# Performance work log

Hardware: AMD Instinct MI355X
Metric: run time of the kernel (lower is better)

Reference implementation:

```python
import jax, jax.numpy as jnp
import numpy as np

N = 50000          # nodes
E = 800000         # edges (avg degree 16)
DIN = 128          # d_input
H = 8              # heads per layer
D = 16             # per-head hidden dim
HID = H * D        # 128
ALPHA = 0.2        # LeakyReLU negative slope in GAT attention
BN_EPS = 1e-5


def _xavier(key, shape):
    fan_in, fan_out = shape[0], shape[-1]
    lim = np.sqrt(6.0 / (fan_in + fan_out)).astype(np.float32)
    return jax.random.uniform(key, shape, jnp.float32, -lim, lim)


def setup_inputs() -> dict:
    key = jax.random.key(0)
    ks = jax.random.split(key, 8)
    x = jax.random.normal(ks[0], (N, DIN), jnp.float32)
    edge_idx = jax.random.randint(ks[1], (2, E), 0, N)
    W1 = _xavier(ks[2], (DIN, HID))
    a1 = _xavier(ks[3], (H, 2 * D))
    W2 = _xavier(ks[4], (HID, HID))
    a2 = _xavier(ks[5], (H, 2 * D))
    W3 = _xavier(ks[6], (HID, HID))
    a3 = _xavier(ks[7], (H, 2 * D))
    ones = jnp.ones((HID,), jnp.float32)
    zeros = jnp.zeros((HID,), jnp.float32)
    return {"x": x, "edge_idx": edge_idx,
            "W1": W1, "a1": a1, "W2": W2, "a2": a2, "W3": W3, "a3": a3,
            "g1": ones, "b1": zeros, "g2": ones, "b2": zeros, "g3": ones, "b3": zeros}


def _leaky(x):
    return jnp.where(x >= 0, x, ALPHA * x)


def _gat_layer(x, src, dst, W, a):
    # x: [N, Fin]; W: [Fin, H*D]; a: [H, 2D]
    h = (x @ W).reshape(-1, H, D)                       # [N, H, D]
    e_src = jnp.einsum('nhd,hd->nh', h, a[:, :D])       # a^T part for source node
    e_dst = jnp.einsum('nhd,hd->nh', h, a[:, D:])       # a^T part for destination node
    e = _leaky(e_src[src] + e_dst[dst])                 # [E, H]
    m = jax.ops.segment_max(e, dst, num_segments=N)     # per-dst stable softmax max
    m = jnp.where(jnp.isfinite(m), m, 0.0)              # empty segments -> 0
    w = jnp.exp(e - m[dst])                             # [E, H]
    den = jax.ops.segment_sum(w, dst, num_segments=N)   # [N, H]
    agg = jax.ops.segment_sum(h[src] * w[:, :, None], dst, num_segments=N)  # [N, H, D]
    out = agg / (den[:, :, None] + 1e-16)
    return out.reshape(-1, HID)                         # concat heads


def _bn(x, g, b):
    # BatchNorm1d training-mode math over the node axis
    mu = x.mean(axis=0)
    var = x.var(axis=0)
    return g * (x - mu) * jax.lax.rsqrt(var + BN_EPS) + b


def reference(x, edge_idx, W1, a1, W2, a2, W3, a3, g1, b1, g2, b2, g3, b3):
    src, dst = edge_idx[0], edge_idx[1]
    h1 = jax.nn.elu(_bn(_gat_layer(x, src, dst, W1, a1), g1, b1))
    h2 = jax.nn.elu(_bn(_gat_layer(h1, src, dst, W2, a2), g2, b2))
    h3_in = h1 + h2  # skip connection
    return _bn(_gat_layer(h3_in, src, dst, W3, a3), g3, b3)
```

## Files before the change

kernel.cpp:

```cpp
#include <hip/hip_runtime.h>
#include <hip/hip_bf16.h>
#include <hip/hip_fp16.h>
#include <cstddef>

#define NNODES 50000
#define NEDGES 800000
#define HID 128
#define NHEAD 8
#define AGG_NB (NNODES / 16)
#define NSLICE 64
#define SLAYER (NSLICE * 512)

#define NBUCK 196
#define BCH 2048
#define BIN_NB ((NEDGES + BCH - 1) / BCH)

typedef __attribute__((ext_vector_type(4))) float floatx4;
typedef _Float16 __attribute__((ext_vector_type(8))) half8;
typedef _Float16 __attribute__((ext_vector_type(2))) half2v;

static inline size_t align_up(size_t x, size_t a) { return (x + a - 1) & ~(a - 1); }

__device__ inline float fexp2(float x) {
#if __has_builtin(__builtin_amdgcn_exp2f)
    return __builtin_amdgcn_exp2f(x);
#else
    return __expf(x * 0.69314718055994531f);
#endif
}

__device__ inline unsigned short f2h(float f) {
    return __builtin_bit_cast(unsigned short, (_Float16)f);
}

__global__ __launch_bounds__(256) void init_kernel(const float* __restrict__ W1,
                                                   const float* __restrict__ W2,
                                                   const float* __restrict__ W3,
                                                   unsigned short* __restrict__ Wt,
                                                   int* __restrict__ zeroA, int nA,
                                                   float* __restrict__ zeroB, int nB) {
    int b = blockIdx.x;
    int t = threadIdx.x;
    if (b < 192) {
        int layer = b >> 6;
        const float* W = (layer == 0) ? W1 : ((layer == 1) ? W2 : W3);
        int idx = (b & 63) * 256 + t;
        int n = idx & 127;
        int k = idx >> 7;
        Wt[layer * 16384 + n * 128 + k] = f2h(W[idx]);
    } else {
        int nb = gridDim.x - 192;
        int bb = b - 192;
        for (int i = bb * 256 + t; i < nA; i += nb * 256) zeroA[i] = 0;
        for (int i = bb * 256 + t; i < nB; i += nb * 256) zeroB[i] = 0.f;
    }
}

__global__ __launch_bounds__(256) void bin_count_kernel(const int* __restrict__ edge,
                                                        int* __restrict__ bucketCnt) {
    __shared__ int h[NBUCK];
    int t = threadIdx.x;
    if (t < NBUCK) h[t] = 0;
    __syncthreads();
    for (int i = blockIdx.x * 256 + t; i < NEDGES; i += gridDim.x * 256)
        atomicAdd(&h[edge[NEDGES + i] >> 8], 1);
    __syncthreads();
    if (t < NBUCK && h[t]) atomicAdd(&bucketCnt[t], h[t]);
}

__global__ __launch_bounds__(256) void bucket_scan_kernel(const int* __restrict__ bucketCnt,
                                                          int* __restrict__ bucketBase) {
    __shared__ int sA[256];
    int t = threadIdx.x;
    int v = (t < NBUCK) ? bucketCnt[t] : 0;
    sA[t] = v;
    __syncthreads();
    for (int off = 1; off < 256; off <<= 1) {
        int x = (t >= off) ? sA[t - off] : 0;
        __syncthreads();
        sA[t] += x;
        __syncthreads();
    }
    if (t < NBUCK) bucketBase[t] = sA[t] - v;
    if (t == 0) bucketBase[NBUCK] = NEDGES;
}

__global__ __launch_bounds__(256) void bin_scatter_kernel(const int* __restrict__ edge,
                                                          const int* __restrict__ bucketBase,
                                                          int* __restrict__ bucketCursor,
                                                          unsigned int* __restrict__ binned) {
    __shared__ int sA[256];
    __shared__ int hcnt[NBUCK];
    __shared__ int hbase[NBUCK];
    __shared__ int gbase[NBUCK];
    __shared__ unsigned int sEnt[BCH];
    __shared__ unsigned char sBk[BCH];
    int t = threadIdx.x;
    int e0 = blockIdx.x * BCH;
    int nv = NEDGES - e0;
    if (nv > BCH) nv = BCH;

    if (t < NBUCK) hcnt[t] = 0;
    __syncthreads();

    int myB[8];
    int myR[8];
    unsigned int myP[8];
    #pragma unroll
    for (int j = 0; j < 8; ++j) {
        int idx = j * 256 + t;
        myB[j] = -1;
        if (idx < nv) {
            int s = edge[e0 + idx];
            int d = edge[NEDGES + e0 + idx];
            int bk = d >> 8;
            myB[j] = bk;
            myP[j] = (unsigned)s | ((unsigned)(d & 255) << 16);
            myR[j] = atomicAdd(&hcnt[bk], 1);
        }
    }
    __syncthreads();
    int hc = (t < NBUCK) ? hcnt[t] : 0;
    sA[t] = hc;
    __syncthreads();
    for (int off = 1; off < 256; off <<= 1) {
        int x = (t >= off) ? sA[t - off] : 0;
        __syncthreads();
        sA[t] += x;
        __syncthreads();
    }
    if (t < NBUCK) {
        hbase[t] = sA[t] - hc;
        gbase[t] = bucketBase[t] + atomicAdd(&bucketCursor[t], hc);
    }
    __syncthreads();
    #pragma unroll
    for (int j = 0; j < 8; ++j) {
        if (myB[j] >= 0) {
            int p = hbase[myB[j]] + myR[j];
            sEnt[p] = myP[j];
            sBk[p] = (unsigned char)myB[j];
        }
    }
    __syncthreads();
    #pragma unroll
    for (int j = 0; j < 8; ++j) {
        int i = j * 256 + t;
        if (i < nv) {
            int bk = sBk[i];
            binned[gbase[bk] + (i - hbase[bk])] = sEnt[i];
        }
    }
}

__global__ __launch_bounds__(256) void fine_csr_kernel(const int* __restrict__ bucketCnt,
                                                       const int* __restrict__ bucketBase,
                                                       const unsigned int* __restrict__ binned,
                                                       int* __restrict__ offs,
                                                       int* __restrict__ csr) {
    __shared__ int sA[256];
    __shared__ int sB[256];
    int t = threadIdx.x;
    int b = blockIdx.x;
    int cntb = bucketCnt[b];
    int base = bucketBase[b];
    sB[t] = 0;
    __syncthreads();
    for (int i = t; i < cntb; i += 256)
        atomicAdd(&sB[(binned[base + i] >> 16) & 255], 1);
    __syncthreads();
    int nc = sB[t];
    sA[t] = nc;
    __syncthreads();
    for (int off = 1; off < 256; off <<= 1) {
        int x = (t >= off) ? sA[t - off] : 0;
        __syncthreads();
        sA[t] += x;
        __syncthreads();
    }
    int nodeBase = base + sA[t] - nc;
    int gid = b * 256 + t;
    if (gid < NNODES) offs[gid] = nodeBase;
    if (b == NBUCK - 1 && t == 0) offs[NNODES] = NEDGES;
    sB[t] = nodeBase;
    __syncthreads();
    for (int i = t; i < cntb; i += 256) {
        unsigned e = binned[base + i];
        int pos = atomicAdd(&sB[(e >> 16) & 255], 1);
        csr[pos] = (int)(e & 0xFFFFu);
    }
}

__global__ __launch_bounds__(256) void bn_finalize_kernel(const float* __restrict__ statsPart,
                                                          const float* __restrict__ g,
                                                          const float* __restrict__ b,
                                                          float* __restrict__ ssv) {
    __shared__ float sm[256];
    int t = threadIdx.x;
    const float* base = statsPart + (t & 127) + ((t >> 7) << 7);
    float s = 0.f;
    #pragma unroll 8
    for (int k = 0; k < NSLICE; ++k) s += base[k * 512];
    sm[t] = s;
    __syncthreads();
    if (t < 128) {
        float mu = sm[t] / (float)NNODES;
        float var = sm[128 + t] / (float)NNODES - mu * mu;
        float rstd = rsqrtf(var + 1e-5f);
        float scale = g[t] * rstd;
        ssv[t] = scale;
        ssv[128 + t] = b[t] - mu * scale;
    }
}

#define GROWS 64
#define ASTRIDE 136
#define LOG2E 1.4426950408889634f
__global__ __launch_bounds__(256) void gemm_kernel(const float* __restrict__ Xin,
                                                   const unsigned short* __restrict__ skip16,
                                                   const float* __restrict__ ssv,
                                                   const unsigned short* __restrict__ Wt,
                                                   const float* __restrict__ a,
                                                   unsigned short* __restrict__ Hw16,
                                                   unsigned short* __restrict__ Hb,
                                                   float* __restrict__ esrc,
                                                   float* __restrict__ edst,
                                                   int mode) {
    __shared__ unsigned short As[GROWS * ASTRIDE];
    __shared__ unsigned short Bs[128 * ASTRIDE];
    int tid = threadIdx.x;
    int rowBase = blockIdx.x * GROWS;

    uint4 breg[8];
    #pragma unroll
    for (int q = 0; q < 8; ++q) {
        int i = q * 256 + tid;
        breg[q] = *(const uint4*)(Wt + (i >> 4) * 128 + (i & 15) * 8);
    }

    int r = tid >> 2;
    int cs = (tid & 3) * 32;
    int gr = rowBase + r;
    bool valid = gr < NNODES;
    float4 vv[8];
    if (valid) {
        #pragma unroll
        for (int j = 0; j < 8; ++j)
            vv[j] = *(const float4*)(Xin + (size_t)gr * HID + cs + j * 4);
    } else {
        #pragma unroll
        for (int j = 0; j < 8; ++j) vv[j] = make_float4(0.f, 0.f, 0.f, 0.f);
    }

    #pragma unroll
    for (int q = 0; q < 8; ++q) {
        int i = q * 256 + tid;
        *(uint4*)(&Bs[(i >> 4) * ASTRIDE + (i & 15) * 8]) = breg[q];
    }

    if (mode >= 1 && valid) {
        uint4 sk[4];
        if (mode == 2) {
            #pragma unroll
            for (int q = 0; q < 4; ++q)
                sk[q] = *(const uint4*)(skip16 + (size_t)gr * HID + cs + q * 8);
        }
        #pragma unroll
        for (int j = 0; j < 8; ++j) {
            int ch = cs + j * 4;
            float4 sc = *(const float4*)(ssv + ch);
            float4 sh = *(const float4*)(ssv + 128 + ch);
            float4 v = vv[j];
            v.x = sc.x * v.x + sh.x;
            v.y = sc.y * v.y + sh.y;
            v.z = sc.z * v.z + sh.z;
            v.w = sc.w * v.w + sh.w;
            v.x = (v.x > 0.f) ? v.x : expm1f(v.x);
            v.y = (v.y > 0.f) ? v.y : expm1f(v.y);
            v.z = (v.z > 0.f) ? v.z : expm1f(v.z);
            v.w = (v.w > 0.f) ? v.w : expm1f(v.w);
            if (mode == 2) {
                const unsigned int* pu = (const unsigned int*)&sk[j >> 1];
                half2v s0 = __builtin_bit_cast(half2v, pu[(j & 1) * 2]);
                half2v s1 = __builtin_bit_cast(half2v, pu[(j & 1) * 2 + 1]);
                v.x += (float)s0[0];
                v.y += (float)s0[1];
                v.z += (float)s1[0];
                v.w += (float)s1[1];
            }
            vv[j] = v;
        }
    }
    {
        unsigned int pk[16];
        #pragma unroll
        for (int j = 0; j < 8; ++j) {
            pk[2 * j]     = __builtin_bit_cast(unsigned int,
                                __builtin_amdgcn_cvt_pkrtz(vv[j].x, vv[j].y));
            pk[2 * j + 1] = __builtin_bit_cast(unsigned int,
                                __builtin_amdgcn_cvt_pkrtz(vv[j].z, vv[j].w));
        }
        if (mode == 1 && valid) {
            #pragma unroll
            for (int q = 0; q < 4; ++q)
                *(uint4*)(Hw16 + (size_t)gr * HID + cs + q * 8) =
                    make_uint4(pk[4 * q], pk[4 * q + 1], pk[4 * q + 2], pk[4 * q + 3]);
        }
        #pragma unroll
        for (int q = 0; q < 4; ++q)
            *(uint4*)(&As[r * ASTRIDE + cs + q * 8]) =
                make_uint4(pk[4 * q], pk[4 * q + 1], pk[4 * q + 2], pk[4 * q + 3]);
    }

    __syncthreads();

    int wv = tid >> 6;
    int lane = tid & 63;
    int l15 = lane & 15;
    int quad = lane >> 4;
    const unsigned short* Arow = &As[(wv * 16 + l15) * ASTRIDE + quad * 8];
    half8 af[4];
    #pragma unroll
    for (int c = 0; c < 4; ++c) af[c] = *(const half8*)(Arow + c * 32);

    floatx4 acc[8];
    #pragma unroll
    for (int h = 0; h < 8; ++h) {
        acc[h] = (floatx4){0.f, 0.f, 0.f, 0.f};
        const unsigned short* Brow = &Bs[(h * 16 + l15) * ASTRIDE + quad * 8];
        #pragma unroll
        for (int c = 0; c < 4; ++c) {
            half8 bfr = *(const half8*)(Brow + c * 32);
            acc[h] = __builtin_amdgcn_mfma_f32_16x16x32_f16(af[c], bfr, acc[h], 0, 0, 0);
        }
    }

    #pragma unroll
    for (int h = 0; h < 8; ++h) {
        #pragma unroll
        for (int reg = 0; reg < 4; ++reg)
            As[(wv * 16 + quad * 4 + reg) * ASTRIDE + h * 16 + l15] = f2h(acc[h][reg]);
    }

    {
        int rr = tid >> 2;
        int hp = tid & 3;
        int grr = rowBase + rr;
        const unsigned short* row = &As[rr * ASTRIDE + hp * 32];
        uint4 u[4];
        #pragma unroll
        for (int q = 0; q < 4; ++q) u[q] = *(const uint4*)(row + q * 8);
        if (grr < NNODES) {
            uint4* dst = (uint4*)(Hb + (size_t)grr * HID + hp * 32);
            #pragma unroll
            for (int q = 0; q < 4; ++q) dst[q] = u[q];
            float f[32];
            #pragma unroll
            for (int q = 0; q < 4; ++q) {
                unsigned int* pu = (unsigned int*)&u[q];
                #pragma unroll
                for (int j = 0; j < 4; ++j) {
                    half2v hv = __builtin_bit_cast(half2v, pu[j]);
                    f[q * 8 + 2 * j]     = (float)hv[0];
                    f[q * 8 + 2 * j + 1] = (float)hv[1];
                }
            }
            int h0 = hp * 2, h1 = hp * 2 + 1;
            float es0 = 0.f, ev0 = 0.f, es1 = 0.f, ev1 = 0.f;
            #pragma unroll
            for (int j = 0; j < 16; ++j) {
                es0 += f[j] * a[h0 * 32 + j];
                ev0 += f[j] * a[h0 * 32 + 16 + j];
                es1 += f[16 + j] * a[h1 * 32 + j];
                ev1 += f[16 + j] * a[h1 * 32 + 16 + j];
            }
            esrc[grr * NHEAD + h0] = es0 * LOG2E;
            esrc[grr * NHEAD + h1] = es1 * LOG2E;
            edst[grr * NHEAD + h0] = ev0 * LOG2E;
            edst[grr * NHEAD + h1] = ev1 * LOG2E;
        }
    }
}

__global__ __launch_bounds__(256) void aggregate_kernel(const int* __restrict__ offs,
                                                        const int* __restrict__ csr,
                                                        const float* __restrict__ esrc,
                                                        const float* __restrict__ edst,
                                                        const unsigned int* __restrict__ Hb,
                                                        float* __restrict__ out,
                                                        float* __restrict__ statsPart) {
    int tid = threadIdx.x;
    int wv = tid >> 6;
    int lane = tid & 63;
    int grp = lane >> 4;
    int sub = lane & 15;
    int head = sub >> 1;
    int n = blockIdx.x * 16 + wv * 4 + grp;
    int beg = offs[n], end = offs[n + 1];
    float ed = edst[n * NHEAD + head];
    float acc[8];
    #pragma unroll
    for (int q = 0; q < 8; ++q) acc[q] = 0.f;
    float den = 0.f;
    for (int i = beg; i < end; i += 4) {
        int ss[4];
        #pragma unroll
        for (int j = 0; j < 4; ++j)
            ss[j] = csr[min(i + j, end - 1)];
        float ee[4];
        uint4 hh[4];
        #pragma unroll
        for (int j = 0; j < 4; ++j)
            ee[j] = esrc[(unsigned)ss[j] * 8u + (unsigned)head];
        #pragma unroll
        for (int j = 0; j < 4; ++j)
            hh[j] = *(const uint4*)(Hb + (unsigned)ss[j] * 64u + (unsigned)sub * 4u);
        #pragma unroll
        for (int j = 0; j < 4; ++j) {
            float e = ee[j] + ed;
            e = fmaxf(e, 0.2f * e);
            float w = fexp2(e);
            w = (i + j < end) ? w : 0.f;
            den += w;
            half2v h0 = __builtin_bit_cast(half2v, hh[j].x);
            half2v h1 = __builtin_bit_cast(half2v, hh[j].y);
            half2v h2 = __builtin_bit_cast(half2v, hh[j].z);
            half2v h3 = __builtin_bit_cast(half2v, hh[j].w);
            acc[0] += w * (float)h0[0];
            acc[1] += w * (float)h0[1];
            acc[2] += w * (float)h1[0];
            acc[3] += w * (float)h1[1];
            acc[4] += w * (float)h2[0];
            acc[5] += w * (float)h2[1];
            acc[6] += w * (float)h3[0];
            acc[7] += w * (float)h3[1];
        }
    }
    float inv = 1.f / (den + 1e-16f);
    float4 o0 = make_float4(acc[0] * inv, acc[1] * inv, acc[2] * inv, acc[3] * inv);
    float4 o1 = make_float4(acc[4] * inv, acc[5] * inv, acc[6] * inv, acc[7] * inv);
    float* orow = out + (size_t)n * HID + sub * 8;
    *(float4*)orow = o0;
    *(float4*)(orow + 4) = o1;

    __shared__ float sm[16 * 136];
    float* srow = &sm[(wv * 4 + grp) * 136 + sub * 8];
    *(float4*)srow = o0;
    *(float4*)(srow + 4) = o1;
    __syncthreads();
    if (tid < 128) {
        float s = 0.f, s2 = 0.f;
        #pragma unroll
        for (int rr = 0; rr < 16; ++rr) {
            float v = sm[rr * 136 + tid];
            s += v;
            s2 += v * v;
        }
        float* slice = statsPart + (blockIdx.x & (NSLICE - 1)) * 512;
        atomicAdd(&slice[tid], s);
        atomicAdd(&slice[128 + tid], s2);
    }
}

__global__ __launch_bounds__(256) void final_apply_kernel(const float* __restrict__ X,
                                                          const float* __restrict__ ssv,
                                                          float* __restrict__ out) {
    __shared__ float ssm[256];
    int tid = threadIdx.x;
    ssm[tid] = ssv[tid];
    __syncthreads();
    int total4 = NNODES * HID / 4;
    for (int i = blockIdx.x * 256 + tid; i < total4; i += gridDim.x * 256) {
        float4 v = ((const float4*)X)[i];
        int c4 = (i & 31) * 4;
        float4 sc = *(const float4*)(ssm + c4);
        float4 sh = *(const float4*)(ssm + 128 + c4);
        v.x = sc.x * v.x + sh.x;
        v.y = sc.y * v.y + sh.y;
        v.z = sc.z * v.z + sh.z;
        v.w = sc.w * v.w + sh.w;
        ((float4*)out)[i] = v;
    }
}

extern "C" void kernel_launch(void* const* d_in, const int* in_sizes, int n_in,
                              void* d_out, int out_size, void* d_ws, size_t ws_size,
                              hipStream_t stream) {
    const float* x   = (const float*)d_in[0];
    const int* edge  = (const int*)d_in[1];
    const float* W1  = (const float*)d_in[2];
    const float* a1  = (const float*)d_in[3];
    const float* W2  = (const float*)d_in[4];
    const float* a2  = (const float*)d_in[5];
    const float* W3  = (const float*)d_in[6];
    const float* a3  = (const float*)d_in[7];
    const float* g1  = (const float*)d_in[8];
    const float* b1  = (const float*)d_in[9];
    const float* g2  = (const float*)d_in[10];
    const float* b2  = (const float*)d_in[11];
    const float* g3  = (const float*)d_in[12];
    const float* b3  = (const float*)d_in[13];
    float* outp      = (float*)d_out;

    char* p = (char*)d_ws;
    size_t cur = 0;
    auto carve = [&](size_t bytes) {
        void* r = p + cur;
        cur = align_up(cur + bytes, 256);
        return r;
    };
    int*   offs   = (int*)carve((NNODES + 1) * sizeof(int));
    int*   csr    = (int*)carve(NEDGES * sizeof(int));
    unsigned short* wt = (unsigned short*)carve(3 * 16384 * sizeof(unsigned short));
    unsigned short* hb = (unsigned short*)carve((size_t)NNODES * HID * sizeof(unsigned short));
    float* agg    = (float*)carve((size_t)NNODES * HID * sizeof(float));
    unsigned short* h1 = (unsigned short*)carve((size_t)NNODES * HID * sizeof(unsigned short));
    float* esrc   = (float*)carve((size_t)NNODES * NHEAD * sizeof(float));
    float* edst   = (float*)carve((size_t)NNODES * NHEAD * sizeof(float));
    float* stats  = (float*)carve(3 * SLAYER * sizeof(float));
    int*   bcnt   = (int*)carve((3 * NBUCK + 1) * sizeof(int));
    int*   bcur   = bcnt + NBUCK;
    int*   bbase  = bcnt + 2 * NBUCK;
    float* ssv    = (float*)carve(3 * 256 * sizeof(float));
    float* stats1 = stats;
    float* stats2 = stats + SLAYER;
    float* stats3 = stats + 2 * SLAYER;
    float* ssv1 = ssv;
    float* ssv2 = ssv + 256;
    float* ssv3 = ssv + 512;
    unsigned int* binned = (unsigned int*)h1;

    const int GB = (NNODES + GROWS - 1) / GROWS;

    init_kernel<<<256, 256, 0, stream>>>(W1, W2, W3, wt,
                                         bcnt, 2 * NBUCK,
                                         stats, 3 * SLAYER);
    bin_count_kernel<<<256, 256, 0, stream>>>(edge, bcnt);
    bucket_scan_kernel<<<1, 256, 0, stream>>>(bcnt, bbase);
    bin_scatter_kernel<<<BIN_NB, 256, 0, stream>>>(edge, bbase, bcur, binned);
    fine_csr_kernel<<<NBUCK, 256, 0, stream>>>(bcnt, bbase, binned, offs, csr);

    gemm_kernel<<<GB, 256, 0, stream>>>(x, nullptr, nullptr,
                                        wt, a1, nullptr, hb, esrc, edst, 0);
    aggregate_kernel<<<AGG_NB, 256, 0, stream>>>(offs, csr, esrc, edst,
                                                 (const unsigned int*)hb, agg, stats1);
    bn_finalize_kernel<<<1, 256, 0, stream>>>(stats1, g1, b1, ssv1);

    gemm_kernel<<<GB, 256, 0, stream>>>(agg, nullptr, ssv1,
                                        wt + 16384, a2, h1, hb, esrc, edst, 1);
    aggregate_kernel<<<AGG_NB, 256, 0, stream>>>(offs, csr, esrc, edst,
                                                 (const unsigned int*)hb, agg, stats2);
    bn_finalize_kernel<<<1, 256, 0, stream>>>(stats2, g2, b2, ssv2);

    gemm_kernel<<<GB, 256, 0, stream>>>(agg, h1, ssv2,
                                        wt + 32768, a3, nullptr, hb, esrc, edst, 2);
    aggregate_kernel<<<AGG_NB, 256, 0, stream>>>(offs, csr, esrc, edst,
                                                 (const unsigned int*)hb, agg, stats3);
    bn_finalize_kernel<<<1, 256, 0, stream>>>(stats3, g3, b3, ssv3);

    final_apply_kernel<<<768, 256, 0, stream>>>(agg, ssv3, outp);
}
```

Measured before the change: 373.4 us.

## Merge bucket scan into scatter, co-launch scatter with layer-1 GEMM, fold final BN finalize

Removes the single-block bucket scan kernel. The scatter and fine-CSR blocks now each recompute the bucket prefix scan locally. The edge-binning scatter and the first-layer GEMM run as one launch with a block-index split, so the independent CSR build overlaps the GEMM. The last BN finalize is folded into the final apply kernel, where every block re-reduces the stats. Together this cuts three launches and their serialization gaps, at the cost of redundant scans and reductions, and the shared-memory footprint is sized to the larger of the two co-launched workloads.

```diff
diff --git a/kernel.cpp b/kernel.cpp
--- a/kernel.cpp
+++ b/kernel.cpp
@@ -14,6 +14,11 @@
 #define NBUCK 196
 #define BCH 2048
 #define BIN_NB ((NEDGES + BCH - 1) / BCH)
+
+#define GROWS 64
+#define ASTRIDE 136
+#define SMEM_BYTES 52224
+#define LOG2E 1.4426950408889634f
 
 typedef __attribute__((ext_vector_type(4))) float floatx4;
 typedef _Float16 __attribute__((ext_vector_type(8))) half8;
@@ -68,12 +73,23 @@
     if (t < NBUCK && h[t]) atomicAdd(&bucketCnt[t], h[t]);
 }
 
-__global__ __launch_bounds__(256) void bucket_scan_kernel(const int* __restrict__ bucketCnt,
-                                                          int* __restrict__ bucketBase) {
-    __shared__ int sA[256];
-    int t = threadIdx.x;
-    int v = (t < NBUCK) ? bucketCnt[t] : 0;
-    sA[t] = v;
+__device__ __forceinline__ void scatter_block(char* smemraw, int bid, int t,
+                                              const int* __restrict__ edge,
+                                              const int* __restrict__ bucketCnt,
+                                              int* __restrict__ bucketCursor,
+                                              unsigned int* __restrict__ binned) {
+    int* sA = (int*)smemraw;
+    int* hcnt = sA + 256;
+    int* hbase = hcnt + 196;
+    int* gbase = hbase + 196;
+    unsigned int* sEnt = (unsigned int*)(gbase + 196);
+    unsigned char* sBk = (unsigned char*)(sEnt + 2048);
+    int e0 = bid * BCH;
+    int nv = NEDGES - e0;
+    if (nv > BCH) nv = BCH;
+
+    int gcnt = (t < NBUCK) ? bucketCnt[t] : 0;
+    sA[t] = gcnt;
     __syncthreads();
     for (int off = 1; off < 256; off <<= 1) {
         int x = (t >= off) ? sA[t - off] : 0;
@@ -81,25 +97,7 @@
         sA[t] += x;
         __syncthreads();
     }
-    if (t < NBUCK) bucketBase[t] = sA[t] - v;
-    if (t == 0) bucketBase[NBUCK] = NEDGES;
-}
-
-__global__ __launch_bounds__(256) void bin_scatter_kernel(const int* __restrict__ edge,
-                                                          const int* __restrict__ bucketBase,
-                                                          int* __restrict__ bucketCursor,
-                                                          unsigned int* __restrict__ binned) {
-    __shared__ int sA[256];
-    __shared__ int hcnt[NBUCK];
-    __shared__ int hbase[NBUCK];
-    __shared__ int gbase[NBUCK];
-    __shared__ unsigned int sEnt[BCH];
-    __shared__ unsigned char sBk[BCH];
-    int t = threadIdx.x;
-    int e0 = blockIdx.x * BCH;
-    int nv = NEDGES - e0;
-    if (nv > BCH) nv = BCH;
-
+    int gExBase = sA[t] - gcnt;
     if (t < NBUCK) hcnt[t] = 0;
     __syncthreads();
 
@@ -131,7 +129,7 @@
     }
     if (t < NBUCK) {
         hbase[t] = sA[t] - hc;
-        gbase[t] = bucketBase[t] + atomicAdd(&bucketCursor[t], hc);
+        gbase[t] = gExBase + atomicAdd(&bucketCursor[t], hc);
     }
     __syncthreads();
     #pragma unroll
@@ -154,7 +152,6 @@
 }
 
 __global__ __launch_bounds__(256) void fine_csr_kernel(const int* __restrict__ bucketCnt,
-                                                       const int* __restrict__ bucketBase,
                                                        const unsigned int* __restrict__ binned,
                                                        int* __restrict__ offs,
                                                        int* __restrict__ csr) {
@@ -162,8 +159,17 @@
     __shared__ int sB[256];
     int t = threadIdx.x;
     int b = blockIdx.x;
+    int v = (t < NBUCK) ? bucketCnt[t] : 0;
+    sA[t] = v;
+    __syncthreads();
+    for (int off = 1; off < 256; off <<= 1) {
+        int x = (t >= off) ? sA[t - off] : 0;
+        __syncthreads();
+        sA[t] += x;
+        __syncthreads();
+    }
     int cntb = bucketCnt[b];
-    int base = bucketBase[b];
+    int base = sA[b] - cntb;
     sB[t] = 0;
     __syncthreads();
     for (int i = t; i < cntb; i += 256)
@@ -213,23 +219,20 @@
     }
 }
 
-#define GROWS 64
-#define ASTRIDE 136
-#define LOG2E 1.4426950408889634f
-__global__ __launch_bounds__(256) void gemm_kernel(const float* __restrict__ Xin,
-                                                   const unsigned short* __restrict__ skip16,
-                                                   const float* __restrict__ ssv,
-                                                   const unsigned short* __restrict__ Wt,
-                                                   const float* __restrict__ a,
-                                                   unsigned short* __restrict__ Hw16,
-                                                   unsigned short* __restrict__ Hb,
-                                                   float* __restrict__ esrc,
-                                                   float* __restrict__ edst,
-                                                   int mode) {
-    __shared__ unsigned short As[GROWS * ASTRIDE];
-    __shared__ unsigned short Bs[128 * ASTRIDE];
-    int tid = threadIdx.x;
-    int rowBase = blockIdx.x * GROWS;
+__device__ __forceinline__ void gemm_block(char* smemraw, int bid, int tid,
+                                           const float* __restrict__ Xin,
+                                           const unsigned short* __restrict__ skip16,
+                                           const float* __restrict__ ssv,
+                                           const unsigned short* __restrict__ Wt,
+                                           const float* __restrict__ a,
+                                           unsigned short* __restrict__ Hw16,
+                                           unsigned short* __restrict__ Hb,
+                                           float* __restrict__ esrc,
+                                           float* __restrict__ edst,
+                                           int mode) {
+    unsigned short* As = (unsigned short*)smemraw;
+    unsigned short* Bs = As + GROWS * ASTRIDE;
+    int rowBase = bid * GROWS;
 
     uint4 breg[8];
     #pragma unroll
@@ -382,6 +385,41 @@
     }
 }
 
+__global__ __launch_bounds__(256) void gemm_kernel(const float* __restrict__ Xin,
+                                                   const unsigned short* __restrict__ skip16,
+                                                   const float* __restrict__ ssv,
+                                                   const unsigned short* __restrict__ Wt,
+                                                   const float* __restrict__ a,
+                                                   unsigned short* __restrict__ Hw16,
+                                                   unsigned short* __restrict__ Hb,
+                                                   float* __restrict__ esrc,
+                                                   float* __restrict__ edst,
+                                                   int mode) {
+    __shared__ char smem[SMEM_BYTES];
+    gemm_block(smem, blockIdx.x, threadIdx.x, Xin, skip16, ssv, Wt, a,
+               Hw16, Hb, esrc, edst, mode);
+}
+
+__global__ __launch_bounds__(256) void gemm1_scatter_kernel(const float* __restrict__ Xin,
+                                                            const unsigned short* __restrict__ Wt,
+                                                            const float* __restrict__ a,
+                                                            unsigned short* __restrict__ Hb,
+                                                            float* __restrict__ esrc,
+                                                            float* __restrict__ edst,
+                                                            const int* __restrict__ edge,
+                                                            const int* __restrict__ bucketCnt,
+                                                            int* __restrict__ bucketCursor,
+                                                            unsigned int* __restrict__ binned) {
+    __shared__ char smem[SMEM_BYTES];
+    int b = blockIdx.x;
+    if (b < BIN_NB) {
+        scatter_block(smem, b, threadIdx.x, edge, bucketCnt, bucketCursor, binned);
+    } else {
+        gemm_block(smem, b - BIN_NB, threadIdx.x, Xin, nullptr, nullptr, Wt, a,
+                   nullptr, Hb, esrc, edst, 0);
+    }
+}
+
 __global__ __launch_bounds__(256) void aggregate_kernel(const int* __restrict__ offs,
                                                         const int* __restrict__ csr,
                                                         const float* __restrict__ esrc,
@@ -463,11 +501,29 @@
 }
 
 __global__ __launch_bounds__(256) void final_apply_kernel(const float* __restrict__ X,
-                                                          const float* __restrict__ ssv,
+                                                          const float* __restrict__ statsPart,
+                                                          const float* __restrict__ g,
+                                                          const float* __restrict__ b,
                                                           float* __restrict__ out) {
     __shared__ float ssm[256];
     int tid = threadIdx.x;
-    ssm[tid] = ssv[tid];
+    {
+        const float* base = statsPart + (tid & 127) + ((tid >> 7) << 7);
+        float s = 0.f;
+        #pragma unroll 8
+        for (int k = 0; k < NSLICE; ++k) s += base[k * 512];
+        ssm[tid] = s;
+    }
+    __syncthreads();
+    if (tid < 128) {
+        float mu = ssm[tid] / (float)NNODES;
+        float var = ssm[128 + tid] / (float)NNODES - mu * mu;
+        float rstd = rsqrtf(var + 1e-5f);
+        float scale = g[tid] * rstd;
+        float shift = b[tid] - mu * scale;
+        ssm[tid] = scale;
+        ssm[128 + tid] = shift;
+    }
     __syncthreads();
     int total4 = NNODES * HID / 4;
     for (int i = blockIdx.x * 256 + tid; i < total4; i += gridDim.x * 256) {
@@ -518,16 +574,14 @@
     float* esrc   = (float*)carve((size_t)NNODES * NHEAD * sizeof(float));
     float* edst   = (float*)carve((size_t)NNODES * NHEAD * sizeof(float));
     float* stats  = (float*)carve(3 * SLAYER * sizeof(float));
-    int*   bcnt   = (int*)carve((3 * NBUCK + 1) * sizeof(int));
+    int*   bcnt   = (int*)carve(2 * NBUCK * sizeof(int));
     int*   bcur   = bcnt + NBUCK;
-    int*   bbase  = bcnt + 2 * NBUCK;
-    float* ssv    = (float*)carve(3 * 256 * sizeof(float));
+    float* ssv    = (float*)carve(2 * 256 * sizeof(float));
     float* stats1 = stats;
     float* stats2 = stats + SLAYER;
     float* stats3 = stats + 2 * SLAYER;
     float* ssv1 = ssv;
     float* ssv2 = ssv + 256;
-    float* ssv3 = ssv + 512;
     unsigned int* binned = (unsigned int*)h1;
 
     const int GB = (NNODES + GROWS - 1) / GROWS;
@@ -536,12 +590,11 @@
                                          bcnt, 2 * NBUCK,
                                          stats, 3 * SLAYER);
     bin_count_kernel<<<256, 256, 0, stream>>>(edge, bcnt);
-    bucket_scan_kernel<<<1, 256, 0, stream>>>(bcnt, bbase);
-    bin_scatter_kernel<<<BIN_NB, 256, 0, stream>>>(edge, bbase, bcur, binned);
-    fine_csr_kernel<<<NBUCK, 256, 0, stream>>>(bcnt, bbase, binned, offs, csr);
-
-    gemm_kernel<<<GB, 256, 0, stream>>>(x, nullptr, nullptr,
-                                        wt, a1, nullptr, hb, esrc, edst, 0);
+
+    gemm1_scatter_kernel<<<BIN_NB + GB, 256, 0, stream>>>(x, wt, a1, hb, esrc, edst,
+                                                          edge, bcnt, bcur, binned);
+    fine_csr_kernel<<<NBUCK, 256, 0, stream>>>(bcnt, binned, offs, csr);
+
     aggregate_kernel<<<AGG_NB, 256, 0, stream>>>(offs, csr, esrc, edst,
                                                  (const unsigned int*)hb, agg, stats1);
     bn_finalize_kernel<<<1, 256, 0, stream>>>(stats1, g1, b1, ssv1);
@@ -556,7 +609,6 @@
                                         wt + 32768, a3, nullptr, hb, esrc, edst, 2);
     aggregate_kernel<<<AGG_NB, 256, 0, stream>>>(offs, csr, esrc, edst,
                                                  (const unsigned int*)hb, agg, stats3);
-    bn_finalize_kernel<<<1, 256, 0, stream>>>(stats3, g3, b3, ssv3);
-
-    final_apply_kernel<<<768, 256, 0, stream>>>(agg, ssv3, outp);
-}
+
+    final_apply_kernel<<<768, 256, 0, stream>>>(agg, stats3, g3, b3, outp);
+}
```

New measurement: 342.4 us. 1.09x faster.
